# Optimization experiments

Measured on AMD Instinct MI355X. Metric: run time of the kernel, lower is better.

The kernel has to match this reference:

```python
import jax, jax.numpy as jnp
import numpy as np

NUM_CLS = 80
TOPK = 100
CONF_THRESH = 0.05
NMS_THRESH = 0.5
NKS_ALPHA = 0.6
INPUT_SIZE = (512, 512)  # (H, W)
STRIDES = (4, 8, 16, 32)
BATCH = 8


def _make_pixel_location():
    H, W = INPUT_SIZE
    locs = []
    for s in STRIDES:
        hs, ws = H // s, W // s
        ys, xs = np.meshgrid(np.arange(hs), np.arange(ws), indexing='ij')
        x = xs * s + s / 2.0
        y = ys * s + s / 2.0
        locs.append(np.stack([x, y, x, y], -1).reshape(-1, 4))
    return np.concatenate(locs, 0).astype(np.float32)  # [HW, 4]


def setup_inputs() -> dict:
    key = jax.random.key(0)
    pix = jnp.asarray(_make_pixel_location())
    HW = pix.shape[0]
    pred_head = jax.random.normal(key, (BATCH, HW, NUM_CLS + 5), dtype=jnp.float32)
    return {"pred_head": pred_head, "pixel_location": pix}


def _nms_single(boxes, scores, cls, valid):
    """Greedy per-class NMS on fixed-size TOPK candidates. Returns keep mask in original order."""
    N = scores.shape[0]
    order = jnp.argsort(-jnp.where(valid, scores, -jnp.inf))
    b = boxes[order]
    v = valid[order]
    c = cls[order]
    x1, y1, x2, y2 = b[:, 0], b[:, 1], b[:, 2], b[:, 3]
    areas = (x2 - x1) * (y2 - y1)
    xx1 = jnp.maximum(x1[:, None], x1[None, :])
    yy1 = jnp.maximum(y1[:, None], y1[None, :])
    xx2 = jnp.minimum(x2[:, None], x2[None, :])
    yy2 = jnp.minimum(y2[:, None], y2[None, :])
    w = jnp.maximum(1e-28, xx2 - xx1)
    h = jnp.maximum(1e-28, yy2 - yy1)
    inter = w * h
    ovr = inter / (areas[:, None] + areas[None, :] - inter)
    # original NMS is per-class: cross-class pairs never suppress
    ovr = jnp.where(c[:, None] == c[None, :], ovr, 0.0)
    idx = jnp.arange(N)

    def body(i, state):
        keep, sup = state
        ki = v[i] & jnp.logical_not(sup[i])
        keep = keep.at[i].set(ki)
        sup = sup | (ki & (ovr[i] > NMS_THRESH) & (idx > i))
        return (keep, sup)

    keep_sorted, _ = jax.lax.fori_loop(0, N, body, (jnp.zeros(N, bool), jnp.zeros(N, bool)))
    return jnp.zeros(N, bool).at[order].set(keep_sorted)


def reference(pred_head, pixel_location):
    B, HW, _ = pred_head.shape
    cls_pred = jax.nn.sigmoid(pred_head[:, :, :NUM_CLS])               # [B, HW, C]
    loc_w = jnp.array([[-1.0, -1.0, 1.0, 1.0]], dtype=pred_head.dtype)
    loc_pred = jax.nn.relu(pred_head[:, :, NUM_CLS:-1]) * loc_w + pixel_location[None]  # [B, HW, 4]
    nks = jax.nn.sigmoid(pred_head[:, :, -1:])
    nks = 1.0 / (1.0 + jnp.exp(-2.0 * nks + 1.0))
    cls_pred = jnp.power(cls_pred, (2.0 - nks) * NKS_ALPHA + 1e-14)

    def pool3x3(x):
        # torch F.max_pool2d on 3D [B,HW,C] pools 3x3 over the (HW, C) plane
        return jax.lax.reduce_window(x, -jnp.inf, jax.lax.max, (1, 3, 3), (1, 1, 1), 'SAME')

    def step(cmap, i):
        # original re-suppresses the shared heatmap on every batch iteration
        hmax = pool3x3(cmap)
        cmap = cmap * (hmax == cmap).astype(cmap.dtype)
        flat = jnp.transpose(cmap[i], (1, 0)).reshape(-1)  # class-major [C*HW], matches permute(1,0).view(-1)
        s, ind = jax.lax.top_k(flat, TOPK)
        return cmap, (s, ind)

    _, (topk_scores, topk_inds) = jax.lax.scan(step, cls_pred, jnp.arange(B))  # [B, TOPK]
    topk_cls = (topk_inds // HW).astype(jnp.int32)
    topk_hw = topk_inds % HW
    boxes = jnp.take_along_axis(loc_pred, topk_hw[:, :, None], axis=1)  # [B, TOPK, 4]
    valid = topk_scores > CONF_THRESH
    keep = jax.vmap(_nms_single)(boxes, topk_scores, topk_cls, valid)   # [B, TOPK] bool
    scale = jnp.array([INPUT_SIZE[1], INPUT_SIZE[0], INPUT_SIZE[1], INPUT_SIZE[0]], dtype=boxes.dtype)
    bboxes = jnp.clip(boxes / scale, 0.0, 1.0)
    return bboxes, topk_scores, topk_cls, keep
```

## Files before the change

kernel.cpp:

```cpp
#include <hip/hip_runtime.h>
#include <math.h>

#define BATCH   8
#define HW      21760
#define NCLS    80
#define NCH     85
#define TOPK    100
#define CAPA    8192
#define CAPB    16384
#define ABUF    256
#define CBUF    512
#define XTH     2.40f
#define STH     0x3F700000u
#define HI_BITS 0x3F75C28Fu
#define LTH     (-0.09315f)
#define RPB     128
#define TILES   170
#define F4PB    2720
#define SORTN   256
#define FBIN    256
#define FSH     12
#define CSTRIDE 64

#define LOG2E 1.44269504088896340736f
__device__ __forceinline__ float xsig(float x) { return 1.0f / (1.0f + expf(-x)); }
__device__ __forceinline__ float exact_score(const float* __restrict__ row, int c) {
    float p  = xsig(row[c]);
    float s1 = xsig(row[NCH - 1]);
    float n2 = 1.0f / (1.0f + expf(1.0f - 2.0f * s1));
    float e  = (2.0f - n2) * 0.6f + 1e-14f;
    return powf(p, e);
}
__device__ __forceinline__ float alog(float x, float en) {
    return en * __builtin_amdgcn_logf(1.0f + __builtin_amdgcn_exp2f(-LOG2E * x));
}
__device__ __forceinline__ float apxeneg(float x) {
    float s1 = __builtin_amdgcn_rcpf(1.0f + __builtin_amdgcn_exp2f(-LOG2E * x));
    float n2 = __builtin_amdgcn_rcpf(1.0f + __builtin_amdgcn_exp2f(-LOG2E * (2.0f * s1 - 1.0f)));
    return -((2.0f - n2) * 0.6f + 1e-14f);
}

__global__ __launch_bounds__(256, 4) void k1_screen(const float* __restrict__ pred,
                                                    float* __restrict__ cvalA, int* __restrict__ cidxA,
                                                    float* __restrict__ cvalB, int* __restrict__ cidxB,
                                                    unsigned int* __restrict__ cnts,
                                                    unsigned int* __restrict__ ghist) {
    int blk = blockIdx.x;
    int b = blk / TILES, tile = blk - b * TILES;
    int hw0 = tile * RPB;
    int tid = threadIdx.x, lane = tid & 63;
    __shared__ float eneg[RPB + 2];
    __shared__ int   scand[CBUF];
    __shared__ int   aidx[ABUF];
    __shared__ unsigned int scn, acnt, shA, shB, gA_s, gB_s;

    float hx = 0.0f;
    if (tid < 2) {
        int hwg = (tid == 0) ? hw0 - 1 : hw0 + RPB;
        hwg = hwg < 0 ? 0 : (hwg > HW - 1 ? HW - 1 : hwg);
        hx = pred[((size_t)b * HW + hwg) * NCH + (NCH - 1)];
    }

    const float4* base4 = (const float4*)(pred + ((size_t)b * HW + hw0) * NCH);
    float4 r[11];
    #pragma unroll
    for (int j = 0; j < 10; ++j) r[j] = base4[tid + j * 256];
    bool t10 = tid < (F4PB - 2560);
    r[10] = base4[t10 ? tid + 2560 : tid];

    if (tid == 0) { scn = 0; acnt = 0; shA = 0; shB = 0; }
    if (tid < 2) eneg[tid == 0 ? 0 : RPB + 1] = apxeneg(hx);
    __syncthreads();

    #pragma unroll
    for (int j = 0; j < 11; ++j) {
        bool active = (j < 10) | t10;
        int v = (j < 10) ? tid + j * 256 : (t10 ? tid + 2560 : tid);
        int f0 = v * 4;
        int m = f0 % 85;
        float4 rj = r[j];
        if (active && m >= 81) {
            int q = 84 - m;
            float x = q == 0 ? rj.x : (q == 1 ? rj.y : (q == 2 ? rj.z : rj.w));
            int i = (f0 - m) / 85;
            eneg[i + 1] = apxeneg(x);
        }
        if (active) {
            #pragma unroll
            for (int q = 0; q < 4; ++q) {
                float x = q == 0 ? rj.x : (q == 1 ? rj.y : (q == 2 ? rj.z : rj.w));
                if (x >= XTH) {
                    int f = f0 + q;
                    int i0 = f / 85, ch = f - i0 * 85;
                    if (ch < NCLS) {
                        unsigned int pos = atomicAdd(&scn, 1u);
                        if (pos < CBUF) scand[pos] = ((i0 + 1) << 7) | ch;
                    }
                }
            }
        }
    }
    __syncthreads();
    unsigned int sn = scn < CBUF ? scn : CBUF;

    for (unsigned int k = tid; k < sn; k += 256) {
        int pk = scand[k];
        int i = pk >> 7, c = pk & 127;
        int cm = c > 0 ? c - 1 : 0, cp = c < NCLS - 1 ? c + 1 : NCLS - 1;
        int h0 = hw0 + i - 2; h0 = h0 < 0 ? 0 : h0;
        int h1 = hw0 + i - 1;
        int h2 = hw0 + i; h2 = h2 > HW - 1 ? HW - 1 : h2;
        const float* r0 = pred + (size_t)(b * HW + h0) * NCH;
        const float* r1 = pred + (size_t)(b * HW + h1) * NCH;
        const float* r2 = pred + (size_t)(b * HW + h2) * NCH;
        float x00 = r0[cm], x01 = r0[c], x02 = r0[cp];
        float x10 = r1[cm], x11 = r1[c], x12 = r1[cp];
        float x20 = r2[cm], x21 = r2[c], x22 = r2[cp];
        float e0 = eneg[i - 1], e1 = eneg[i], e2 = eneg[i + 1];
        float l00 = alog(x00, e0), l01 = alog(x01, e0), l02 = alog(x02, e0);
        float l10 = alog(x10, e1), l11 = alog(x11, e1), l12 = alog(x12, e1);
        float l20 = alog(x20, e2), l21 = alog(x21, e2), l22 = alog(x22, e2);
        float mx = fmaxf(fmaxf(fmaxf(fmaxf(l00, l01), fmaxf(l02, l10)),
                               fmaxf(fmaxf(l11, l12), fmaxf(l20, l21))), l22);
        float lv = l11;
        bool adm = (lv >= mx) && (lv >= LTH);
        unsigned long long mb = __ballot(adm);
        if (mb) {
            int ldr = __ffsll(mb) - 1;
            unsigned int base = 0;
            if (lane == ldr) base = atomicAdd(&acnt, (unsigned int)__popcll(mb));
            base = (unsigned int)__shfl((int)base, ldr);
            if (adm) {
                unsigned int pos = base + (unsigned int)__popcll(mb & ((1ULL << lane) - 1ULL));
                int gi = c * HW + hw0 + i - 1;
                if (pos < ABUF) aidx[pos] = gi;
                else {
                    int hw = gi - c * HW;
                    float v2 = exact_score(pred + ((size_t)b * HW + hw) * NCH, c);
                    unsigned int bits2 = __float_as_uint(v2);
                    unsigned int rel2 = bits2 >= STH ? bits2 - STH : 0u;
                    unsigned int bin2 = rel2 >> FSH; if (bin2 > FBIN - 1) bin2 = FBIN - 1;
                    atomicAdd(&ghist[b * FBIN + bin2], 1u);
                    if (bits2 >= HI_BITS) {
                        unsigned int g = atomicAdd(&cnts[b * CSTRIDE + 0], 1u);
                        if (g < CAPA) { cvalA[b * CAPA + g] = v2; cidxA[b * CAPA + g] = gi; }
                        else { unsigned int g2 = atomicAdd(&cnts[b * CSTRIDE + 1], 1u);
                               if (g2 < CAPB) { cvalB[b * CAPB + g2] = v2; cidxB[b * CAPB + g2] = gi; } }
                    } else {
                        unsigned int g2 = atomicAdd(&cnts[b * CSTRIDE + 1], 1u);
                        if (g2 < CAPB) { cvalB[b * CAPB + g2] = v2; cidxB[b * CAPB + g2] = gi; }
                    }
                }
            }
        }
    }
    __syncthreads();

    unsigned int nb = acnt < ABUF ? acnt : ABUF;
    float ve = 0.0f; int gi = 0; unsigned int pos = 0; bool isA = false;
    bool act = tid < (int)nb;
    if (act) {
        gi = aidx[tid];
        int c = gi / HW, hw = gi - c * HW;
        ve = exact_score(pred + ((size_t)b * HW + hw) * NCH, c);
        unsigned int bits = __float_as_uint(ve);
        unsigned int rel = bits >= STH ? bits - STH : 0u;
        unsigned int bin = rel >> FSH; if (bin > FBIN - 1) bin = FBIN - 1;
        atomicAdd(&ghist[b * FBIN + bin], 1u);
        isA = bits >= HI_BITS;
        pos = atomicAdd(isA ? &shA : &shB, 1u);
    }
    __syncthreads();
    if (tid == 0) {
        if (shA) gA_s = atomicAdd(&cnts[b * CSTRIDE + 0], shA);
        if (shB) gB_s = atomicAdd(&cnts[b * CSTRIDE + 1], shB);
    }
    __syncthreads();
    if (act) {
        if (isA) {
            unsigned int gp = gA_s + pos;
            if (gp < CAPA) { cvalA[b * CAPA + gp] = ve; cidxA[b * CAPA + gp] = gi; }
            else { unsigned int g2 = atomicAdd(&cnts[b * CSTRIDE + 1], 1u);
                   if (g2 < CAPB) { cvalB[b * CAPB + g2] = ve; cidxB[b * CAPB + g2] = gi; } }
        } else {
            unsigned int gp = gB_s + pos;
            if (gp < CAPB) { cvalB[b * CAPB + gp] = ve; cidxB[b * CAPB + gp] = gi; }
        }
    }
}

#define KFT 512
__global__ __launch_bounds__(KFT) void k_final(const float* __restrict__ pred, const float* __restrict__ pix,
                                               const float* __restrict__ cvalA, const int* __restrict__ cidxA,
                                               const float* __restrict__ cvalB, const int* __restrict__ cidxB,
                                               const unsigned int* __restrict__ cnts,
                                               const unsigned int* __restrict__ ghist,
                                               float* __restrict__ out) {
    int b = blockIdx.x;
    int tid = threadIdx.x;
    unsigned int cA_raw = cnts[b * CSTRIDE + 0];
    unsigned int cB_raw = cnts[b * CSTRIDE + 1];
    int cntA = (int)(cA_raw < CAPA ? cA_raw : CAPA);
    int cntB = (int)(cB_raw < CAPB ? cB_raw : CAPB);

    __shared__ unsigned int sfx[FBIN];
    __shared__ unsigned int fbmax, m;
    __shared__ unsigned long long kv[SORTN];
    if (tid < FBIN) sfx[tid] = ghist[b * FBIN + tid];
    if (tid < SORTN) kv[tid] = 0ULL;
    if (tid == 0) { fbmax = 0; m = 0; }
    __syncthreads();
    #pragma unroll
    for (int s = 1; s < FBIN; s <<= 1) {
        unsigned int v = (tid + s < FBIN) ? sfx[tid + s] : 0u;
        __syncthreads();
        if (tid < FBIN) sfx[tid] += v;
        __syncthreads();
    }
    if (tid < FBIN && sfx[tid] >= TOPK) atomicMax(&fbmax, (unsigned int)tid);
    __syncthreads();
    unsigned int edge = STH + (fbmax << FSH);
    bool scanB = (edge < HI_BITS) || (cA_raw > CAPA);

    for (int k = tid; k < cntA; k += KFT) {
        unsigned int bits = __float_as_uint(cvalA[b * CAPA + k]);
        if (bits >= edge) {
            unsigned int p2 = atomicAdd(&m, 1u);
            if (p2 < SORTN)
                kv[p2] = ((unsigned long long)bits << 32) | (unsigned int)(~(unsigned int)cidxA[b * CAPA + k]);
        }
    }
    if (scanB) {
        for (int k = tid; k < cntB; k += KFT) {
            unsigned int bits = __float_as_uint(cvalB[b * CAPB + k]);
            if (bits >= edge) {
                unsigned int p2 = atomicAdd(&m, 1u);
                if (p2 < SORTN)
                    kv[p2] = ((unsigned long long)bits << 32) | (unsigned int)(~(unsigned int)cidxB[b * CAPB + k]);
            }
        }
    }
    __syncthreads();

    for (unsigned int kk = 2; kk <= SORTN; kk <<= 1) {
        for (unsigned int j = kk >> 1; j > 0; j >>= 1) {
            if (tid < SORTN) {
                unsigned int i = (unsigned int)tid;
                unsigned int ixj = i ^ j;
                if (ixj > i) {
                    unsigned long long a = kv[i], bq = kv[ixj];
                    bool sw = ((i & kk) == 0) ? (a < bq) : (a > bq);
                    if (sw) { kv[i] = bq; kv[ixj] = a; }
                }
            }
            __syncthreads();
        }
    }

    __shared__ float tv[TOPK];
    __shared__ int   ti[TOPK];
    if (tid < TOPK) {
        unsigned long long kq = kv[tid];
        if (kq == 0ULL) { tv[tid] = 0.0f; ti[tid] = 0; }
        else {
            tv[tid] = __uint_as_float((unsigned int)(kq >> 32));
            ti[tid] = (int)(~(unsigned int)kq);
        }
    }
    __syncthreads();

    __shared__ float x1s[TOPK], y1s[TOPK], x2s[TOPK], y2s[TOPK], ar[TOPK];
    __shared__ int cls[TOPK];
    __shared__ unsigned int ovb[TOPK][4];
    __shared__ unsigned int valm[4], keepm[4];
    for (int t = tid; t < TOPK * 4; t += KFT) ovb[t >> 2][t & 3] = 0;
    if (tid < 4) { valm[tid] = 0; keepm[tid] = 0; }
    __syncthreads();
    if (tid < TOPK) {
        int k = tid;
        int idx = ti[k];
        int c = idx / HW, hw = idx - c * HW;
        const float* p = pred + ((size_t)(b * HW + hw)) * NCH + NCLS;
        float a0 = fmaxf(p[0], 0.0f), a1 = fmaxf(p[1], 0.0f);
        float a2 = fmaxf(p[2], 0.0f), a3 = fmaxf(p[3], 0.0f);
        float px = pix[hw * 4 + 0], py = pix[hw * 4 + 1];
        float X1 = px - a0, Y1 = py - a1, X2 = px + a2, Y2 = py + a3;
        x1s[k] = X1; y1s[k] = Y1; x2s[k] = X2; y2s[k] = Y2;
        ar[k] = (X2 - X1) * (Y2 - Y1);
        cls[k] = c;
        if (tv[k] > 0.05f) atomicOr(&valm[k >> 5], 1u << (k & 31));
    }
    __syncthreads();

    for (int t = tid; t < TOPK * TOPK; t += KFT) {
        int i = t / TOPK, j = t - i * TOPK;
        if (j > i && cls[i] == cls[j]) {
            float xx1 = fmaxf(x1s[i], x1s[j]), yy1 = fmaxf(y1s[i], y1s[j]);
            float xx2 = fminf(x2s[i], x2s[j]), yy2 = fminf(y2s[i], y2s[j]);
            float w = fmaxf(1e-28f, xx2 - xx1), h = fmaxf(1e-28f, yy2 - yy1);
            float inter = w * h;
            float ovr = inter / (ar[i] + ar[j] - inter);
            if (ovr > 0.5f) atomicOr(&ovb[i][j >> 5], 1u << (j & 31));
        }
    }
    __syncthreads();

    if (tid == 0) {
        unsigned int sup0 = 0, sup1 = 0, sup2 = 0, sup3 = 0;
        unsigned int km0 = 0, km1 = 0, km2 = 0, km3 = 0;
        for (int i = 0; i < TOPK; ++i) {
            unsigned int w = i >> 5, bit = 1u << (i & 31);
            unsigned int supw = w == 0 ? sup0 : (w == 1 ? sup1 : (w == 2 ? sup2 : sup3));
            bool ki = ((valm[w] & bit) != 0) && ((supw & bit) == 0);
            if (ki) {
                if (w == 0) km0 |= bit; else if (w == 1) km1 |= bit; else if (w == 2) km2 |= bit; else km3 |= bit;
                sup0 |= ovb[i][0]; sup1 |= ovb[i][1]; sup2 |= ovb[i][2]; sup3 |= ovb[i][3];
            }
        }
        keepm[0] = km0; keepm[1] = km1; keepm[2] = km2; keepm[3] = km3;
    }
    __syncthreads();

    if (tid < TOPK) {
        int k = tid;
        const float inv = 1.0f / 512.0f;
        float b0 = fminf(fmaxf(x1s[k] * inv, 0.0f), 1.0f);
        float b1 = fminf(fmaxf(y1s[k] * inv, 0.0f), 1.0f);
        float b2 = fminf(fmaxf(x2s[k] * inv, 0.0f), 1.0f);
        float b3 = fminf(fmaxf(y2s[k] * inv, 0.0f), 1.0f);
        size_t o = (size_t)b * TOPK + k;
        out[o * 4 + 0] = b0; out[o * 4 + 1] = b1;
        out[o * 4 + 2] = b2; out[o * 4 + 3] = b3;
        out[(size_t)BATCH * TOPK * 4 + o] = tv[k];
        out[(size_t)BATCH * TOPK * 5 + o] = (float)cls[k];
        out[(size_t)BATCH * TOPK * 6 + o] = ((keepm[k >> 5] >> (k & 31)) & 1u) ? 1.0f : 0.0f;
    }
}

extern "C" void kernel_launch(void* const* d_in, const int* in_sizes, int n_in,
                              void* d_out, int out_size, void* d_ws, size_t ws_size,
                              hipStream_t stream) {
    const float* pred = (const float*)d_in[0];
    const float* pix  = (const float*)d_in[1];
    float* out = (float*)d_out;

    char* ws = (char*)d_ws;
    size_t off = 0;
    unsigned int* cnts  = (unsigned int*)(ws + off); off += (size_t)BATCH * CSTRIDE * sizeof(unsigned int);
    unsigned int* ghist = (unsigned int*)(ws + off); off += (size_t)BATCH * FBIN * sizeof(unsigned int);
    size_t zero_bytes = off;
    off = (off + 255) & ~(size_t)255;
    float* cvalA = (float*)(ws + off);               off += (size_t)BATCH * CAPA * sizeof(float);
    int*   cidxA = (int*)(ws + off);                 off += (size_t)BATCH * CAPA * sizeof(int);
    float* cvalB = (float*)(ws + off);               off += (size_t)BATCH * CAPB * sizeof(float);
    int*   cidxB = (int*)(ws + off);                 off += (size_t)BATCH * CAPB * sizeof(int);

    hipMemsetAsync(cnts, 0, zero_bytes, stream);

    k1_screen<<<BATCH * TILES, 256, 0, stream>>>(pred, cvalA, cidxA, cvalB, cidxB, cnts, ghist);
    k_final  <<<BATCH,         KFT, 0, stream>>>(pred, pix, cvalA, cidxA, cvalB, cidxB, cnts, ghist, out);
}
```

Measured before the change: 136.2 us.

## Stage screen tiles in LDS via async global_load_lds and halve rows per block

The screening kernel now copies each tile of prediction rows, plus one halo row on each side, straight into shared memory with global_load_lds instead of holding it in registers. The 3x3 neighbourhood reads and the exact score evaluation then come from LDS rather than re-reading global memory. Rows per block drop from 128 to 64, doubling the grid, and the two per-batch counters are packed into one 64-bit atomic so they can be reserved together. The block also skips per-element checks when a float4's maximum is below the threshold. In exchange it uses about 22KB of LDS per block, which may limit occupancy, and it depends on the lane-ordered layout of global_load_lds.

```diff
diff --git a/kernel.cpp b/kernel.cpp
--- a/kernel.cpp
+++ b/kernel.cpp
@@ -14,9 +14,11 @@
 #define STH     0x3F700000u
 #define HI_BITS 0x3F75C28Fu
 #define LTH     (-0.09315f)
-#define RPB     128
-#define TILES   170
-#define F4PB    2720
+#define RPB     64
+#define TILES   340
+#define F4PB    1360
+#define HALO_LO 5440
+#define HALO_HI 5525
 #define SORTN   256
 #define FBIN    256
 #define FSH     12
@@ -24,7 +26,7 @@
 
 #define LOG2E 1.44269504088896340736f
 __device__ __forceinline__ float xsig(float x) { return 1.0f / (1.0f + expf(-x)); }
-__device__ __forceinline__ float exact_score(const float* __restrict__ row, int c) {
+__device__ __forceinline__ float exact_score_lds(const float* row, int c) {
     float p  = xsig(row[c]);
     float s1 = xsig(row[NCH - 1]);
     float n2 = 1.0f / (1.0f + expf(1.0f - 2.0f * s1));
@@ -40,61 +42,79 @@
     return -((2.0f - n2) * 0.6f + 1e-14f);
 }
 
-__global__ __launch_bounds__(256, 4) void k1_screen(const float* __restrict__ pred,
-                                                    float* __restrict__ cvalA, int* __restrict__ cidxA,
-                                                    float* __restrict__ cvalB, int* __restrict__ cidxB,
-                                                    unsigned int* __restrict__ cnts,
-                                                    unsigned int* __restrict__ ghist) {
+typedef const __attribute__((address_space(1))) void* gas_ptr;
+typedef __attribute__((address_space(3))) void* las_ptr;
+
+__global__ __launch_bounds__(256) void k1_screen(const float* __restrict__ pred,
+                                                 float* __restrict__ cvalA, int* __restrict__ cidxA,
+                                                 float* __restrict__ cvalB, int* __restrict__ cidxB,
+                                                 unsigned long long* __restrict__ cnts64,
+                                                 unsigned int* __restrict__ ghist) {
     int blk = blockIdx.x;
     int b = blk / TILES, tile = blk - b * TILES;
     int hw0 = tile * RPB;
     int tid = threadIdx.x, lane = tid & 63;
+
+    __shared__ float lds_tile[5610];
     __shared__ float eneg[RPB + 2];
     __shared__ int   scand[CBUF];
     __shared__ int   aidx[ABUF];
-    __shared__ unsigned int scn, acnt, shA, shB, gA_s, gB_s;
-
-    float hx = 0.0f;
-    if (tid < 2) {
-        int hwg = (tid == 0) ? hw0 - 1 : hw0 + RPB;
+    __shared__ unsigned int scn, acnt, shA, shB;
+    __shared__ unsigned long long gAB;
+
+    if (tid == 0) { scn = 0; acnt = 0; shA = 0; shB = 0; }
+
+    const float* gbase = pred + ((size_t)b * HW + hw0) * NCH;
+    int wid6 = tid & ~63;
+    #pragma unroll
+    for (int j = 0; j < 6; ++j) {
+        int f4 = j * 256 + tid;
+        if (f4 < F4PB) {
+            __builtin_amdgcn_global_load_lds(
+                (gas_ptr)(const void*)(gbase + (size_t)f4 * 4),
+                (las_ptr)(void*)(lds_tile + (size_t)(j * 256 + wid6) * 4),
+                16, 0, 0);
+        }
+    }
+    if (tid < 170) {
+        int r = tid / 85, c0 = tid - r * 85;
+        int hwg = (r == 0) ? hw0 - 1 : hw0 + RPB;
         hwg = hwg < 0 ? 0 : (hwg > HW - 1 ? HW - 1 : hwg);
-        hx = pred[((size_t)b * HW + hwg) * NCH + (NCH - 1)];
-    }
-
-    const float4* base4 = (const float4*)(pred + ((size_t)b * HW + hw0) * NCH);
-    float4 r[11];
+        lds_tile[(r == 0 ? HALO_LO : HALO_HI) + c0] = pred[((size_t)b * HW + hwg) * NCH + c0];
+    }
+    __syncthreads();
+
+    if (tid < RPB + 2) {
+        int r = tid - 1;
+        int off = (r < 0) ? HALO_LO : (r > RPB - 1 ? HALO_HI : r * NCH);
+        eneg[tid] = apxeneg(lds_tile[off + 84]);
+    }
+
+    int m0 = (tid * 4) % 85;
+    int ib = (tid * 4) / 85;
+    __syncthreads();
+
     #pragma unroll
-    for (int j = 0; j < 10; ++j) r[j] = base4[tid + j * 256];
-    bool t10 = tid < (F4PB - 2560);
-    r[10] = base4[t10 ? tid + 2560 : tid];
-
-    if (tid == 0) { scn = 0; acnt = 0; shA = 0; shB = 0; }
-    if (tid < 2) eneg[tid == 0 ? 0 : RPB + 1] = apxeneg(hx);
-    __syncthreads();
-
-    #pragma unroll
-    for (int j = 0; j < 11; ++j) {
-        bool active = (j < 10) | t10;
-        int v = (j < 10) ? tid + j * 256 : (t10 ? tid + 2560 : tid);
-        int f0 = v * 4;
-        int m = f0 % 85;
-        float4 rj = r[j];
-        if (active && m >= 81) {
-            int q = 84 - m;
-            float x = q == 0 ? rj.x : (q == 1 ? rj.y : (q == 2 ? rj.z : rj.w));
-            int i = (f0 - m) / 85;
-            eneg[i + 1] = apxeneg(x);
-        }
-        if (active) {
-            #pragma unroll
-            for (int q = 0; q < 4; ++q) {
-                float x = q == 0 ? rj.x : (q == 1 ? rj.y : (q == 2 ? rj.z : rj.w));
-                if (x >= XTH) {
-                    int f = f0 + q;
-                    int i0 = f / 85, ch = f - i0 * 85;
-                    if (ch < NCLS) {
-                        unsigned int pos = atomicAdd(&scn, 1u);
-                        if (pos < CBUF) scand[pos] = ((i0 + 1) << 7) | ch;
+    for (int j = 0; j < 6; ++j) {
+        int f4 = j * 256 + tid;
+        if (f4 < F4PB) {
+            const float4 rj = *reinterpret_cast<const float4*>(lds_tile + (size_t)f4 * 4);
+            int mr = m0 + 4 * j;
+            int w  = mr >= 85 ? 1 : 0;
+            int mj = mr - (w ? 85 : 0);
+            int ij = ib + 12 * j + w;
+            float mx4 = fmaxf(fmaxf(rj.x, rj.y), fmaxf(rj.z, rj.w));
+            if (mx4 >= XTH) {
+                #pragma unroll
+                for (int q = 0; q < 4; ++q) {
+                    float x = q == 0 ? rj.x : (q == 1 ? rj.y : (q == 2 ? rj.z : rj.w));
+                    if (x >= XTH) {
+                        int ch = mj + q, row = ij;
+                        if (ch >= 85) { ch -= 85; ++row; }
+                        if (ch < NCLS) {
+                            unsigned int pos = atomicAdd(&scn, 1u);
+                            if (pos < CBUF) scand[pos] = ((row + 1) << 7) | ch;
+                        }
                     }
                 }
             }
@@ -106,16 +126,14 @@
     for (unsigned int k = tid; k < sn; k += 256) {
         int pk = scand[k];
         int i = pk >> 7, c = pk & 127;
+        int li = i - 1;
         int cm = c > 0 ? c - 1 : 0, cp = c < NCLS - 1 ? c + 1 : NCLS - 1;
-        int h0 = hw0 + i - 2; h0 = h0 < 0 ? 0 : h0;
-        int h1 = hw0 + i - 1;
-        int h2 = hw0 + i; h2 = h2 > HW - 1 ? HW - 1 : h2;
-        const float* r0 = pred + (size_t)(b * HW + h0) * NCH;
-        const float* r1 = pred + (size_t)(b * HW + h1) * NCH;
-        const float* r2 = pred + (size_t)(b * HW + h2) * NCH;
-        float x00 = r0[cm], x01 = r0[c], x02 = r0[cp];
-        float x10 = r1[cm], x11 = r1[c], x12 = r1[cp];
-        float x20 = r2[cm], x21 = r2[c], x22 = r2[cp];
+        int o0 = (li - 1 < 0) ? HALO_LO : (li - 1) * NCH;
+        int o1 = li * NCH;
+        int o2 = (li + 1 > RPB - 1) ? HALO_HI : (li + 1) * NCH;
+        float x00 = lds_tile[o0 + cm], x01 = lds_tile[o0 + c], x02 = lds_tile[o0 + cp];
+        float x10 = lds_tile[o1 + cm], x11 = lds_tile[o1 + c], x12 = lds_tile[o1 + cp];
+        float x20 = lds_tile[o2 + cm], x21 = lds_tile[o2 + c], x22 = lds_tile[o2 + cp];
         float e0 = eneg[i - 1], e1 = eneg[i], e2 = eneg[i + 1];
         float l00 = alog(x00, e0), l01 = alog(x01, e0), l02 = alog(x02, e0);
         float l10 = alog(x10, e1), l11 = alog(x11, e1), l12 = alog(x12, e1);
@@ -132,22 +150,22 @@
             base = (unsigned int)__shfl((int)base, ldr);
             if (adm) {
                 unsigned int pos = base + (unsigned int)__popcll(mb & ((1ULL << lane) - 1ULL));
-                int gi = c * HW + hw0 + i - 1;
+                int gi = c * HW + hw0 + li;
                 if (pos < ABUF) aidx[pos] = gi;
                 else {
-                    int hw = gi - c * HW;
-                    float v2 = exact_score(pred + ((size_t)b * HW + hw) * NCH, c);
+                    float v2 = exact_score_lds(lds_tile + (size_t)li * NCH, c);
                     unsigned int bits2 = __float_as_uint(v2);
                     unsigned int rel2 = bits2 >= STH ? bits2 - STH : 0u;
                     unsigned int bin2 = rel2 >> FSH; if (bin2 > FBIN - 1) bin2 = FBIN - 1;
                     atomicAdd(&ghist[b * FBIN + bin2], 1u);
                     if (bits2 >= HI_BITS) {
-                        unsigned int g = atomicAdd(&cnts[b * CSTRIDE + 0], 1u);
+                        unsigned long long og = atomicAdd(&cnts64[b * (CSTRIDE / 2)], 1ull);
+                        unsigned int g = (unsigned int)og;
                         if (g < CAPA) { cvalA[b * CAPA + g] = v2; cidxA[b * CAPA + g] = gi; }
-                        else { unsigned int g2 = atomicAdd(&cnts[b * CSTRIDE + 1], 1u);
+                        else { unsigned int g2 = (unsigned int)(atomicAdd(&cnts64[b * (CSTRIDE / 2)], 1ull << 32) >> 32);
                                if (g2 < CAPB) { cvalB[b * CAPB + g2] = v2; cidxB[b * CAPB + g2] = gi; } }
                     } else {
-                        unsigned int g2 = atomicAdd(&cnts[b * CSTRIDE + 1], 1u);
+                        unsigned int g2 = (unsigned int)(atomicAdd(&cnts64[b * (CSTRIDE / 2)], 1ull << 32) >> 32);
                         if (g2 < CAPB) { cvalB[b * CAPB + g2] = v2; cidxB[b * CAPB + g2] = gi; }
                     }
                 }
@@ -162,7 +180,8 @@
     if (act) {
         gi = aidx[tid];
         int c = gi / HW, hw = gi - c * HW;
-        ve = exact_score(pred + ((size_t)b * HW + hw) * NCH, c);
+        int li = hw - hw0;
+        ve = exact_score_lds(lds_tile + (size_t)li * NCH, c);
         unsigned int bits = __float_as_uint(ve);
         unsigned int rel = bits >= STH ? bits - STH : 0u;
         unsigned int bin = rel >> FSH; if (bin > FBIN - 1) bin = FBIN - 1;
@@ -171,16 +190,17 @@
         pos = atomicAdd(isA ? &shA : &shB, 1u);
     }
     __syncthreads();
-    if (tid == 0) {
-        if (shA) gA_s = atomicAdd(&cnts[b * CSTRIDE + 0], shA);
-        if (shB) gB_s = atomicAdd(&cnts[b * CSTRIDE + 1], shB);
+    if (tid == 0 && (shA | shB)) {
+        gAB = atomicAdd(&cnts64[b * (CSTRIDE / 2)],
+                        ((unsigned long long)shB << 32) | (unsigned long long)shA);
     }
     __syncthreads();
     if (act) {
+        unsigned int gA_s = (unsigned int)gAB, gB_s = (unsigned int)(gAB >> 32);
         if (isA) {
             unsigned int gp = gA_s + pos;
             if (gp < CAPA) { cvalA[b * CAPA + gp] = ve; cidxA[b * CAPA + gp] = gi; }
-            else { unsigned int g2 = atomicAdd(&cnts[b * CSTRIDE + 1], 1u);
+            else { unsigned int g2 = (unsigned int)(atomicAdd(&cnts64[b * (CSTRIDE / 2)], 1ull << 32) >> 32);
                    if (g2 < CAPB) { cvalB[b * CAPB + g2] = ve; cidxB[b * CAPB + g2] = gi; } }
         } else {
             unsigned int gp = gB_s + pos;
@@ -193,13 +213,14 @@
 __global__ __launch_bounds__(KFT) void k_final(const float* __restrict__ pred, const float* __restrict__ pix,
                                                const float* __restrict__ cvalA, const int* __restrict__ cidxA,
                                                const float* __restrict__ cvalB, const int* __restrict__ cidxB,
-                                               const unsigned int* __restrict__ cnts,
+                                               const unsigned long long* __restrict__ cnts64,
                                                const unsigned int* __restrict__ ghist,
                                                float* __restrict__ out) {
     int b = blockIdx.x;
     int tid = threadIdx.x;
-    unsigned int cA_raw = cnts[b * CSTRIDE + 0];
-    unsigned int cB_raw = cnts[b * CSTRIDE + 1];
+    unsigned long long cc = cnts64[b * (CSTRIDE / 2)];
+    unsigned int cA_raw = (unsigned int)cc;
+    unsigned int cB_raw = (unsigned int)(cc >> 32);
     int cntA = (int)(cA_raw < CAPA ? cA_raw : CAPA);
     int cntB = (int)(cB_raw < CAPB ? cB_raw : CAPB);
 
@@ -346,7 +367,8 @@
 
     char* ws = (char*)d_ws;
     size_t off = 0;
-    unsigned int* cnts  = (unsigned int*)(ws + off); off += (size_t)BATCH * CSTRIDE * sizeof(unsigned int);
+    unsigned long long* cnts64 = (unsigned long long*)(ws + off);
+    off += (size_t)BATCH * CSTRIDE * sizeof(unsigned int);
     unsigned int* ghist = (unsigned int*)(ws + off); off += (size_t)BATCH * FBIN * sizeof(unsigned int);
     size_t zero_bytes = off;
     off = (off + 255) & ~(size_t)255;
@@ -355,8 +377,8 @@
     float* cvalB = (float*)(ws + off);               off += (size_t)BATCH * CAPB * sizeof(float);
     int*   cidxB = (int*)(ws + off);                 off += (size_t)BATCH * CAPB * sizeof(int);
 
-    hipMemsetAsync(cnts, 0, zero_bytes, stream);
-
-    k1_screen<<<BATCH * TILES, 256, 0, stream>>>(pred, cvalA, cidxA, cvalB, cidxB, cnts, ghist);
-    k_final  <<<BATCH,         KFT, 0, stream>>>(pred, pix, cvalA, cidxA, cvalB, cidxB, cnts, ghist, out);
-}
+    hipMemsetAsync(cnts64, 0, zero_bytes, stream);
+
+    k1_screen<<<BATCH * TILES, 256, 0, stream>>>(pred, cvalA, cidxA, cvalB, cidxB, cnts64, ghist);
+    k_final  <<<BATCH,         KFT, 0, stream>>>(pred, pix, cvalA, cidxA, cvalB, cidxB, cnts64, ghist, out);
+}
```

Measured after the change: 141.8 us. +4.1%, slower.

## Make screening kernel wave-independent with per-wave slots and packed 64-bit counters

Applied to the files above, without the earlier changes.

Restructures the screening kernel so each 64-lane wave owns 16 rows and runs on its own. Candidates are compacted with ballots into per-wave LDS slots, which removes all block-level barriers and shared atomics. Neighbour exponents are recomputed from global loads instead of being kept in a shared eneg array. The A/B output counters are merged into one 64-bit atomic issued once per wave. The cost is redundant reads of column 84 and extra transcendental math per candidate, plus reliance on an inline waitcnt instead of a barrier for intra-wave LDS visibility.

```diff
diff --git a/kernel.cpp b/kernel.cpp
--- a/kernel.cpp
+++ b/kernel.cpp
@@ -8,25 +8,22 @@
 #define TOPK    100
 #define CAPA    8192
 #define CAPB    16384
-#define ABUF    256
-#define CBUF    512
 #define XTH     2.40f
 #define STH     0x3F700000u
 #define HI_BITS 0x3F75C28Fu
 #define LTH     (-0.09315f)
-#define RPB     128
-#define TILES   170
-#define F4PB    2720
+#define RPW     16
+#define WPB_TOT 1360
+#define WSLOT   128
 #define SORTN   256
 #define FBIN    256
 #define FSH     12
 #define CSTRIDE 64
 
 #define LOG2E 1.44269504088896340736f
-__device__ __forceinline__ float xsig(float x) { return 1.0f / (1.0f + expf(-x)); }
-__device__ __forceinline__ float exact_score(const float* __restrict__ row, int c) {
-    float p  = xsig(row[c]);
-    float s1 = xsig(row[NCH - 1]);
+__device__ __forceinline__ float exact_from(float xc, float x84) {
+    float p  = 1.0f / (1.0f + expf(-xc));
+    float s1 = 1.0f / (1.0f + expf(-x84));
     float n2 = 1.0f / (1.0f + expf(1.0f - 2.0f * s1));
     float e  = (2.0f - n2) * 0.6f + 1e-14f;
     return powf(p, e);
@@ -43,147 +40,107 @@
 __global__ __launch_bounds__(256, 4) void k1_screen(const float* __restrict__ pred,
                                                     float* __restrict__ cvalA, int* __restrict__ cidxA,
                                                     float* __restrict__ cvalB, int* __restrict__ cidxB,
-                                                    unsigned int* __restrict__ cnts,
+                                                    unsigned long long* __restrict__ cnts64,
                                                     unsigned int* __restrict__ ghist) {
-    int blk = blockIdx.x;
-    int b = blk / TILES, tile = blk - b * TILES;
-    int hw0 = tile * RPB;
-    int tid = threadIdx.x, lane = tid & 63;
-    __shared__ float eneg[RPB + 2];
-    __shared__ int   scand[CBUF];
-    __shared__ int   aidx[ABUF];
-    __shared__ unsigned int scn, acnt, shA, shB, gA_s, gB_s;
-
-    float hx = 0.0f;
-    if (tid < 2) {
-        int hwg = (tid == 0) ? hw0 - 1 : hw0 + RPB;
-        hwg = hwg < 0 ? 0 : (hwg > HW - 1 ? HW - 1 : hwg);
-        hx = pred[((size_t)b * HW + hwg) * NCH + (NCH - 1)];
-    }
-
-    const float4* base4 = (const float4*)(pred + ((size_t)b * HW + hw0) * NCH);
-    float4 r[11];
+    int tid = threadIdx.x, lane = tid & 63, w = tid >> 6;
+    int wg = blockIdx.x * 4 + w;
+    int b = wg / WPB_TOT, wsl = wg - b * WPB_TOT;
+    int row0 = wsl * RPW;
+
+    __shared__ int slots[4][WSLOT];
+
+    const float4* g4 = (const float4*)(pred + ((size_t)b * HW + row0) * NCH);
+    float4 r[6];
     #pragma unroll
-    for (int j = 0; j < 10; ++j) r[j] = base4[tid + j * 256];
-    bool t10 = tid < (F4PB - 2560);
-    r[10] = base4[t10 ? tid + 2560 : tid];
-
-    if (tid == 0) { scn = 0; acnt = 0; shA = 0; shB = 0; }
-    if (tid < 2) eneg[tid == 0 ? 0 : RPB + 1] = apxeneg(hx);
-    __syncthreads();
-
+    for (int j = 0; j < 5; ++j) r[j] = g4[lane + j * 64];
+    { int v5 = lane + 320; r[5] = g4[v5 < 340 ? v5 : 0]; }
+    bool v5ok = lane < 20;
+
+    int m0 = lane * 4, rl = 0;
+    if (m0 >= 170) { m0 -= 170; rl = 2; } else if (m0 >= 85) { m0 -= 85; rl = 1; }
+    unsigned int ns = 0;
+    unsigned long long ltm = (1ULL << lane) - 1ULL;
     #pragma unroll
-    for (int j = 0; j < 11; ++j) {
-        bool active = (j < 10) | t10;
-        int v = (j < 10) ? tid + j * 256 : (t10 ? tid + 2560 : tid);
-        int f0 = v * 4;
-        int m = f0 % 85;
+    for (int j = 0; j < 6; ++j) {
         float4 rj = r[j];
-        if (active && m >= 81) {
-            int q = 84 - m;
+        bool act = (j < 5) | v5ok;
+        #pragma unroll
+        for (int q = 0; q < 4; ++q) {
             float x = q == 0 ? rj.x : (q == 1 ? rj.y : (q == 2 ? rj.z : rj.w));
-            int i = (f0 - m) / 85;
-            eneg[i + 1] = apxeneg(x);
-        }
-        if (active) {
-            #pragma unroll
-            for (int q = 0; q < 4; ++q) {
-                float x = q == 0 ? rj.x : (q == 1 ? rj.y : (q == 2 ? rj.z : rj.w));
-                if (x >= XTH) {
-                    int f = f0 + q;
-                    int i0 = f / 85, ch = f - i0 * 85;
-                    if (ch < NCLS) {
-                        unsigned int pos = atomicAdd(&scn, 1u);
-                        if (pos < CBUF) scand[pos] = ((i0 + 1) << 7) | ch;
-                    }
-                }
-            }
-        }
-    }
-    __syncthreads();
-    unsigned int sn = scn < CBUF ? scn : CBUF;
-
-    for (unsigned int k = tid; k < sn; k += 256) {
-        int pk = scand[k];
-        int i = pk >> 7, c = pk & 127;
-        int cm = c > 0 ? c - 1 : 0, cp = c < NCLS - 1 ? c + 1 : NCLS - 1;
-        int h0 = hw0 + i - 2; h0 = h0 < 0 ? 0 : h0;
-        int h1 = hw0 + i - 1;
-        int h2 = hw0 + i; h2 = h2 > HW - 1 ? HW - 1 : h2;
-        const float* r0 = pred + (size_t)(b * HW + h0) * NCH;
-        const float* r1 = pred + (size_t)(b * HW + h1) * NCH;
-        const float* r2 = pred + (size_t)(b * HW + h2) * NCH;
-        float x00 = r0[cm], x01 = r0[c], x02 = r0[cp];
-        float x10 = r1[cm], x11 = r1[c], x12 = r1[cp];
-        float x20 = r2[cm], x21 = r2[c], x22 = r2[cp];
-        float e0 = eneg[i - 1], e1 = eneg[i], e2 = eneg[i + 1];
+            bool hit = false; int pk = 0;
+            if (act && x >= XTH) {
+                int ch = m0 + q, rr = rl;
+                if (ch >= 85) { ch -= 85; ++rr; }
+                if (ch < NCLS) { hit = true; pk = (rr << 7) | ch; }
+            }
+            unsigned long long mb = __ballot(hit);
+            if (mb) {
+                unsigned int pos = ns + (unsigned int)__popcll(mb & ltm);
+                if (hit && pos < WSLOT) slots[w][pos] = pk;
+                ns += (unsigned int)__popcll(mb);
+            }
+        }
+        m0 += 1; rl += 3; if (m0 >= 85) { m0 -= 85; rl += 1; }
+    }
+
+    asm volatile("s_waitcnt lgkmcnt(0)" ::: "memory");
+
+    unsigned int total = ns < WSLOT ? ns : WSLOT;
+    for (unsigned int base = 0; base < total; base += 64) {
+        unsigned int cnt = total - base; if (cnt > 64) cnt = 64;
+        bool act = lane < cnt;
+        int pk = slots[w][base + (act ? lane : 0)];
+        int rr = row0 + (pk >> 7), ch = pk & 127;
+        int h0 = rr - 1 < 0 ? 0 : rr - 1;
+        int h2 = rr + 1 > HW - 1 ? HW - 1 : rr + 1;
+        int cm = ch > 0 ? ch - 1 : 0, cp = ch < NCLS - 1 ? ch + 1 : NCLS - 1;
+        const float* r0p = pred + ((size_t)b * HW + h0) * NCH;
+        const float* r1p = pred + ((size_t)b * HW + rr) * NCH;
+        const float* r2p = pred + ((size_t)b * HW + h2) * NCH;
+        float x00 = r0p[cm], x01 = r0p[ch], x02 = r0p[cp], s84_0 = r0p[84];
+        float x10 = r1p[cm], x11 = r1p[ch], x12 = r1p[cp], s84_1 = r1p[84];
+        float x20 = r2p[cm], x21 = r2p[ch], x22 = r2p[cp], s84_2 = r2p[84];
+        float e0 = apxeneg(s84_0), e1 = apxeneg(s84_1), e2 = apxeneg(s84_2);
         float l00 = alog(x00, e0), l01 = alog(x01, e0), l02 = alog(x02, e0);
         float l10 = alog(x10, e1), l11 = alog(x11, e1), l12 = alog(x12, e1);
         float l20 = alog(x20, e2), l21 = alog(x21, e2), l22 = alog(x22, e2);
         float mx = fmaxf(fmaxf(fmaxf(fmaxf(l00, l01), fmaxf(l02, l10)),
                                fmaxf(fmaxf(l11, l12), fmaxf(l20, l21))), l22);
-        float lv = l11;
-        bool adm = (lv >= mx) && (lv >= LTH);
-        unsigned long long mb = __ballot(adm);
-        if (mb) {
-            int ldr = __ffsll(mb) - 1;
-            unsigned int base = 0;
-            if (lane == ldr) base = atomicAdd(&acnt, (unsigned int)__popcll(mb));
-            base = (unsigned int)__shfl((int)base, ldr);
-            if (adm) {
-                unsigned int pos = base + (unsigned int)__popcll(mb & ((1ULL << lane) - 1ULL));
-                int gi = c * HW + hw0 + i - 1;
-                if (pos < ABUF) aidx[pos] = gi;
-                else {
-                    int hw = gi - c * HW;
-                    float v2 = exact_score(pred + ((size_t)b * HW + hw) * NCH, c);
-                    unsigned int bits2 = __float_as_uint(v2);
-                    unsigned int rel2 = bits2 >= STH ? bits2 - STH : 0u;
-                    unsigned int bin2 = rel2 >> FSH; if (bin2 > FBIN - 1) bin2 = FBIN - 1;
-                    atomicAdd(&ghist[b * FBIN + bin2], 1u);
-                    if (bits2 >= HI_BITS) {
-                        unsigned int g = atomicAdd(&cnts[b * CSTRIDE + 0], 1u);
-                        if (g < CAPA) { cvalA[b * CAPA + g] = v2; cidxA[b * CAPA + g] = gi; }
-                        else { unsigned int g2 = atomicAdd(&cnts[b * CSTRIDE + 1], 1u);
-                               if (g2 < CAPB) { cvalB[b * CAPB + g2] = v2; cidxB[b * CAPB + g2] = gi; } }
-                    } else {
-                        unsigned int g2 = atomicAdd(&cnts[b * CSTRIDE + 1], 1u);
-                        if (g2 < CAPB) { cvalB[b * CAPB + g2] = v2; cidxB[b * CAPB + g2] = gi; }
-                    }
-                }
-            }
-        }
-    }
-    __syncthreads();
-
-    unsigned int nb = acnt < ABUF ? acnt : ABUF;
-    float ve = 0.0f; int gi = 0; unsigned int pos = 0; bool isA = false;
-    bool act = tid < (int)nb;
-    if (act) {
-        gi = aidx[tid];
-        int c = gi / HW, hw = gi - c * HW;
-        ve = exact_score(pred + ((size_t)b * HW + hw) * NCH, c);
-        unsigned int bits = __float_as_uint(ve);
-        unsigned int rel = bits >= STH ? bits - STH : 0u;
-        unsigned int bin = rel >> FSH; if (bin > FBIN - 1) bin = FBIN - 1;
-        atomicAdd(&ghist[b * FBIN + bin], 1u);
-        isA = bits >= HI_BITS;
-        pos = atomicAdd(isA ? &shA : &shB, 1u);
-    }
-    __syncthreads();
-    if (tid == 0) {
-        if (shA) gA_s = atomicAdd(&cnts[b * CSTRIDE + 0], shA);
-        if (shB) gB_s = atomicAdd(&cnts[b * CSTRIDE + 1], shB);
-    }
-    __syncthreads();
-    if (act) {
+        bool adm = act && (l11 >= mx) && (l11 >= LTH);
+
+        float ve = 0.0f; unsigned int bits = 0; int gi = 0;
+        if (adm) {
+            gi = ch * HW + rr;
+            ve = exact_from(x11, s84_1);
+            bits = __float_as_uint(ve);
+            unsigned int rel = bits >= STH ? bits - STH : 0u;
+            unsigned int bin = rel >> FSH; if (bin > FBIN - 1) bin = FBIN - 1;
+            atomicAdd(&ghist[b * FBIN + bin], 1u);
+        }
+        bool isA = adm && (bits >= HI_BITS);
+        bool isB = adm && (bits <  HI_BITS);
+        unsigned long long mbA = __ballot(isA), mbB = __ballot(isB);
+        unsigned int nA = (unsigned int)__popcll(mbA), nB = (unsigned int)__popcll(mbB);
+        unsigned int old_lo = 0, old_hi = 0;
+        if (lane == 0 && (nA | nB)) {
+            unsigned long long old = atomicAdd(&cnts64[b * (CSTRIDE / 2)],
+                                               (unsigned long long)nA | ((unsigned long long)nB << 32));
+            old_lo = (unsigned int)old;
+            old_hi = (unsigned int)(old >> 32);
+        }
+        old_lo = (unsigned int)__shfl((int)old_lo, 0);
+        old_hi = (unsigned int)__shfl((int)old_hi, 0);
+        unsigned int gA = old_lo, gB = old_hi;
         if (isA) {
-            unsigned int gp = gA_s + pos;
+            unsigned int gp = gA + (unsigned int)__popcll(mbA & ltm);
             if (gp < CAPA) { cvalA[b * CAPA + gp] = ve; cidxA[b * CAPA + gp] = gi; }
-            else { unsigned int g2 = atomicAdd(&cnts[b * CSTRIDE + 1], 1u);
-                   if (g2 < CAPB) { cvalB[b * CAPB + g2] = ve; cidxB[b * CAPB + g2] = gi; } }
-        } else {
-            unsigned int gp = gB_s + pos;
+            else {
+                unsigned int g2 = (unsigned int)(atomicAdd(&cnts64[b * (CSTRIDE / 2)], 1ull << 32) >> 32);
+                if (g2 < CAPB) { cvalB[b * CAPB + g2] = ve; cidxB[b * CAPB + g2] = gi; }
+            }
+        }
+        if (isB) {
+            unsigned int gp = gB + (unsigned int)__popcll(mbB & ltm);
             if (gp < CAPB) { cvalB[b * CAPB + gp] = ve; cidxB[b * CAPB + gp] = gi; }
         }
     }
@@ -193,13 +150,14 @@
 __global__ __launch_bounds__(KFT) void k_final(const float* __restrict__ pred, const float* __restrict__ pix,
                                                const float* __restrict__ cvalA, const int* __restrict__ cidxA,
                                                const float* __restrict__ cvalB, const int* __restrict__ cidxB,
-                                               const unsigned int* __restrict__ cnts,
+                                               const unsigned long long* __restrict__ cnts64,
                                                const unsigned int* __restrict__ ghist,
                                                float* __restrict__ out) {
     int b = blockIdx.x;
     int tid = threadIdx.x;
-    unsigned int cA_raw = cnts[b * CSTRIDE + 0];
-    unsigned int cB_raw = cnts[b * CSTRIDE + 1];
+    unsigned long long cc = cnts64[b * (CSTRIDE / 2)];
+    unsigned int cA_raw = (unsigned int)cc;
+    unsigned int cB_raw = (unsigned int)(cc >> 32);
     int cntA = (int)(cA_raw < CAPA ? cA_raw : CAPA);
     int cntB = (int)(cB_raw < CAPB ? cB_raw : CAPB);
 
@@ -346,7 +304,8 @@
 
     char* ws = (char*)d_ws;
     size_t off = 0;
-    unsigned int* cnts  = (unsigned int*)(ws + off); off += (size_t)BATCH * CSTRIDE * sizeof(unsigned int);
+    unsigned long long* cnts64 = (unsigned long long*)(ws + off);
+    off += (size_t)BATCH * CSTRIDE * sizeof(unsigned int);
     unsigned int* ghist = (unsigned int*)(ws + off); off += (size_t)BATCH * FBIN * sizeof(unsigned int);
     size_t zero_bytes = off;
     off = (off + 255) & ~(size_t)255;
@@ -355,8 +314,8 @@
     float* cvalB = (float*)(ws + off);               off += (size_t)BATCH * CAPB * sizeof(float);
     int*   cidxB = (int*)(ws + off);                 off += (size_t)BATCH * CAPB * sizeof(int);
 
-    hipMemsetAsync(cnts, 0, zero_bytes, stream);
-
-    k1_screen<<<BATCH * TILES, 256, 0, stream>>>(pred, cvalA, cidxA, cvalB, cidxB, cnts, ghist);
-    k_final  <<<BATCH,         KFT, 0, stream>>>(pred, pix, cvalA, cidxA, cvalB, cidxB, cnts, ghist, out);
-}
+    hipMemsetAsync(cnts64, 0, zero_bytes, stream);
+
+    k1_screen<<<(BATCH * WPB_TOT) / 4, 256, 0, stream>>>(pred, cvalA, cidxA, cvalB, cidxB, cnts64, ghist);
+    k_final  <<<BATCH,                 KFT, 0, stream>>>(pred, pix, cvalA, cidxA, cvalB, cidxB, cnts64, ghist, out);
+}
```

Result: slower. 163.8 us (+20.3%).

## Replace global atomic candidate lists with per-tile slot buffers and in-kernel histogram

Applied to the files above, without the earlier changes.

The screening kernel now writes each tile's admitted candidates into a fixed 256-slot region per tile, along with a per-tile count. This removes the global atomics, the two-tier A/B candidate buffers, the global histogram and the memset launch. The final kernel builds the score histogram itself in shared memory by scanning all tile slots, then gathers candidates above the threshold. Overflow candidates beyond 256 per tile are now dropped rather than scored, which risks correctness on dense inputs. The final kernel also scans a larger slot space (170×256 per batch) twice using only 8 blocks.

```diff
diff --git a/kernel.cpp b/kernel.cpp
--- a/kernel.cpp
+++ b/kernel.cpp
@@ -6,21 +6,18 @@
 #define NCLS    80
 #define NCH     85
 #define TOPK    100
-#define CAPA    8192
-#define CAPB    16384
 #define ABUF    256
 #define CBUF    512
 #define XTH     2.40f
 #define STH     0x3F700000u
-#define HI_BITS 0x3F75C28Fu
 #define LTH     (-0.09315f)
 #define RPB     128
 #define TILES   170
 #define F4PB    2720
+#define SLOTP   256
 #define SORTN   256
 #define FBIN    256
 #define FSH     12
-#define CSTRIDE 64
 
 #define LOG2E 1.44269504088896340736f
 __device__ __forceinline__ float xsig(float x) { return 1.0f / (1.0f + expf(-x)); }
@@ -41,10 +38,8 @@
 }
 
 __global__ __launch_bounds__(256, 4) void k1_screen(const float* __restrict__ pred,
-                                                    float* __restrict__ cvalA, int* __restrict__ cidxA,
-                                                    float* __restrict__ cvalB, int* __restrict__ cidxB,
-                                                    unsigned int* __restrict__ cnts,
-                                                    unsigned int* __restrict__ ghist) {
+                                                    float* __restrict__ sval, int* __restrict__ sidx,
+                                                    unsigned int* __restrict__ cnt_g) {
     int blk = blockIdx.x;
     int b = blk / TILES, tile = blk - b * TILES;
     int hw0 = tile * RPB;
@@ -52,7 +47,7 @@
     __shared__ float eneg[RPB + 2];
     __shared__ int   scand[CBUF];
     __shared__ int   aidx[ABUF];
-    __shared__ unsigned int scn, acnt, shA, shB, gA_s, gB_s;
+    __shared__ unsigned int scn, acnt;
 
     float hx = 0.0f;
     if (tid < 2) {
@@ -68,7 +63,7 @@
     bool t10 = tid < (F4PB - 2560);
     r[10] = base4[t10 ? tid + 2560 : tid];
 
-    if (tid == 0) { scn = 0; acnt = 0; shA = 0; shB = 0; }
+    if (tid == 0) { scn = 0; acnt = 0; }
     if (tid < 2) eneg[tid == 0 ? 0 : RPB + 1] = apxeneg(hx);
     __syncthreads();
 
@@ -134,81 +129,50 @@
                 unsigned int pos = base + (unsigned int)__popcll(mb & ((1ULL << lane) - 1ULL));
                 int gi = c * HW + hw0 + i - 1;
                 if (pos < ABUF) aidx[pos] = gi;
-                else {
-                    int hw = gi - c * HW;
-                    float v2 = exact_score(pred + ((size_t)b * HW + hw) * NCH, c);
-                    unsigned int bits2 = __float_as_uint(v2);
-                    unsigned int rel2 = bits2 >= STH ? bits2 - STH : 0u;
-                    unsigned int bin2 = rel2 >> FSH; if (bin2 > FBIN - 1) bin2 = FBIN - 1;
-                    atomicAdd(&ghist[b * FBIN + bin2], 1u);
-                    if (bits2 >= HI_BITS) {
-                        unsigned int g = atomicAdd(&cnts[b * CSTRIDE + 0], 1u);
-                        if (g < CAPA) { cvalA[b * CAPA + g] = v2; cidxA[b * CAPA + g] = gi; }
-                        else { unsigned int g2 = atomicAdd(&cnts[b * CSTRIDE + 1], 1u);
-                               if (g2 < CAPB) { cvalB[b * CAPB + g2] = v2; cidxB[b * CAPB + g2] = gi; } }
-                    } else {
-                        unsigned int g2 = atomicAdd(&cnts[b * CSTRIDE + 1], 1u);
-                        if (g2 < CAPB) { cvalB[b * CAPB + g2] = v2; cidxB[b * CAPB + g2] = gi; }
-                    }
-                }
             }
         }
     }
     __syncthreads();
 
     unsigned int nb = acnt < ABUF ? acnt : ABUF;
-    float ve = 0.0f; int gi = 0; unsigned int pos = 0; bool isA = false;
-    bool act = tid < (int)nb;
-    if (act) {
-        gi = aidx[tid];
+    if (tid < (int)nb) {
+        int gi = aidx[tid];
         int c = gi / HW, hw = gi - c * HW;
-        ve = exact_score(pred + ((size_t)b * HW + hw) * NCH, c);
-        unsigned int bits = __float_as_uint(ve);
-        unsigned int rel = bits >= STH ? bits - STH : 0u;
-        unsigned int bin = rel >> FSH; if (bin > FBIN - 1) bin = FBIN - 1;
-        atomicAdd(&ghist[b * FBIN + bin], 1u);
-        isA = bits >= HI_BITS;
-        pos = atomicAdd(isA ? &shA : &shB, 1u);
-    }
-    __syncthreads();
-    if (tid == 0) {
-        if (shA) gA_s = atomicAdd(&cnts[b * CSTRIDE + 0], shA);
-        if (shB) gB_s = atomicAdd(&cnts[b * CSTRIDE + 1], shB);
-    }
-    __syncthreads();
-    if (act) {
-        if (isA) {
-            unsigned int gp = gA_s + pos;
-            if (gp < CAPA) { cvalA[b * CAPA + gp] = ve; cidxA[b * CAPA + gp] = gi; }
-            else { unsigned int g2 = atomicAdd(&cnts[b * CSTRIDE + 1], 1u);
-                   if (g2 < CAPB) { cvalB[b * CAPB + g2] = ve; cidxB[b * CAPB + g2] = gi; } }
-        } else {
-            unsigned int gp = gB_s + pos;
-            if (gp < CAPB) { cvalB[b * CAPB + gp] = ve; cidxB[b * CAPB + gp] = gi; }
-        }
-    }
+        float ve = exact_score(pred + ((size_t)b * HW + hw) * NCH, c);
+        size_t sb = ((size_t)(b * TILES + tile)) * SLOTP + tid;
+        sval[sb] = ve;
+        sidx[sb] = gi;
+    }
+    if (tid == 0) cnt_g[b * TILES + tile] = nb;
 }
 
 #define KFT 512
 __global__ __launch_bounds__(KFT) void k_final(const float* __restrict__ pred, const float* __restrict__ pix,
-                                               const float* __restrict__ cvalA, const int* __restrict__ cidxA,
-                                               const float* __restrict__ cvalB, const int* __restrict__ cidxB,
-                                               const unsigned int* __restrict__ cnts,
-                                               const unsigned int* __restrict__ ghist,
+                                               const float* __restrict__ sval, const int* __restrict__ sidx,
+                                               const unsigned int* __restrict__ cnt_g,
                                                float* __restrict__ out) {
     int b = blockIdx.x;
     int tid = threadIdx.x;
-    unsigned int cA_raw = cnts[b * CSTRIDE + 0];
-    unsigned int cB_raw = cnts[b * CSTRIDE + 1];
-    int cntA = (int)(cA_raw < CAPA ? cA_raw : CAPA);
-    int cntB = (int)(cB_raw < CAPB ? cB_raw : CAPB);
-
+
+    __shared__ unsigned int scnt[TILES];
     __shared__ unsigned int sfx[FBIN];
     __shared__ unsigned int fbmax, m;
     __shared__ unsigned long long kv[SORTN];
-    if (tid < FBIN) sfx[tid] = ghist[b * FBIN + tid];
+    for (int t = tid; t < TILES; t += KFT) scnt[t] = cnt_g[b * TILES + t];
+    if (tid < FBIN) sfx[tid] = 0;
     if (tid < SORTN) kv[tid] = 0ULL;
     if (tid == 0) { fbmax = 0; m = 0; }
+    __syncthreads();
+
+    for (int t = tid; t < TILES * SLOTP; t += KFT) {
+        int blk = t >> 8, s = t & 255;
+        if (s < (int)scnt[blk]) {
+            unsigned int bits = __float_as_uint(sval[((size_t)(b * TILES + blk)) * SLOTP + s]);
+            unsigned int rel = bits >= STH ? bits - STH : 0u;
+            unsigned int bin = rel >> FSH; if (bin > FBIN - 1) bin = FBIN - 1;
+            atomicAdd(&sfx[bin], 1u);
+        }
+    }
     __syncthreads();
     #pragma unroll
     for (int s = 1; s < FBIN; s <<= 1) {
@@ -220,23 +184,16 @@
     if (tid < FBIN && sfx[tid] >= TOPK) atomicMax(&fbmax, (unsigned int)tid);
     __syncthreads();
     unsigned int edge = STH + (fbmax << FSH);
-    bool scanB = (edge < HI_BITS) || (cA_raw > CAPA);
-
-    for (int k = tid; k < cntA; k += KFT) {
-        unsigned int bits = __float_as_uint(cvalA[b * CAPA + k]);
-        if (bits >= edge) {
-            unsigned int p2 = atomicAdd(&m, 1u);
-            if (p2 < SORTN)
-                kv[p2] = ((unsigned long long)bits << 32) | (unsigned int)(~(unsigned int)cidxA[b * CAPA + k]);
-        }
-    }
-    if (scanB) {
-        for (int k = tid; k < cntB; k += KFT) {
-            unsigned int bits = __float_as_uint(cvalB[b * CAPB + k]);
+
+    for (int t = tid; t < TILES * SLOTP; t += KFT) {
+        int blk = t >> 8, s = t & 255;
+        if (s < (int)scnt[blk]) {
+            size_t sb = ((size_t)(b * TILES + blk)) * SLOTP + s;
+            unsigned int bits = __float_as_uint(sval[sb]);
             if (bits >= edge) {
                 unsigned int p2 = atomicAdd(&m, 1u);
                 if (p2 < SORTN)
-                    kv[p2] = ((unsigned long long)bits << 32) | (unsigned int)(~(unsigned int)cidxB[b * CAPB + k]);
+                    kv[p2] = ((unsigned long long)bits << 32) | (unsigned int)(~(unsigned int)sidx[sb]);
             }
         }
     }
@@ -346,17 +303,12 @@
 
     char* ws = (char*)d_ws;
     size_t off = 0;
-    unsigned int* cnts  = (unsigned int*)(ws + off); off += (size_t)BATCH * CSTRIDE * sizeof(unsigned int);
-    unsigned int* ghist = (unsigned int*)(ws + off); off += (size_t)BATCH * FBIN * sizeof(unsigned int);
-    size_t zero_bytes = off;
+    unsigned int* cnt_g = (unsigned int*)(ws + off); off += (size_t)BATCH * TILES * sizeof(unsigned int);
     off = (off + 255) & ~(size_t)255;
-    float* cvalA = (float*)(ws + off);               off += (size_t)BATCH * CAPA * sizeof(float);
-    int*   cidxA = (int*)(ws + off);                 off += (size_t)BATCH * CAPA * sizeof(int);
-    float* cvalB = (float*)(ws + off);               off += (size_t)BATCH * CAPB * sizeof(float);
-    int*   cidxB = (int*)(ws + off);                 off += (size_t)BATCH * CAPB * sizeof(int);
-
-    hipMemsetAsync(cnts, 0, zero_bytes, stream);
-
-    k1_screen<<<BATCH * TILES, 256, 0, stream>>>(pred, cvalA, cidxA, cvalB, cidxB, cnts, ghist);
-    k_final  <<<BATCH,         KFT, 0, stream>>>(pred, pix, cvalA, cidxA, cvalB, cidxB, cnts, ghist, out);
-}
+    float* sval = (float*)(ws + off);                off += (size_t)BATCH * TILES * SLOTP * sizeof(float);
+    int*   sidx = (int*)(ws + off);                  off += (size_t)BATCH * TILES * SLOTP * sizeof(int);
+
+
+    k1_screen<<<BATCH * TILES, 256, 0, stream>>>(pred, sval, sidx, cnt_g);
+    k_final  <<<BATCH,         KFT, 0, stream>>>(pred, pix, sval, sidx, cnt_g, out);
+}
```

New measurement: 185.1 us. +35.9%, slower.
